# Performance work log

Hardware: AMD Instinct MI355X
Metric: run time of the kernel (lower is better)

Reference implementation:

```python
import jax, jax.numpy as jnp
import numpy as np

B, N, K = 4, 32768, 16
IN_DIM, HID, OUT_DIM = 32, 64, 32
N_DIM = 2
KIN = 2 * N_DIM + OUT_DIM  # 36
KH = 64
EPS = 1e-5


def _gelu(x):
    return jax.nn.gelu(x, approximate=False)  # torch F.gelu default (erf)


def setup_inputs() -> dict:
    key = jax.random.key(0)
    ks = jax.random.split(key, 16)
    s = lambda fan_in: 1.0 / np.sqrt(fan_in)
    return {
        "inp": jax.random.normal(ks[0], (B, N, IN_DIM), jnp.float32),
        "input_grid": jax.random.uniform(ks[1], (N, N_DIM), jnp.float32),
        "output_grid": jax.random.uniform(ks[2], (N, N_DIM), jnp.float32),
        "neighbor_idx": jax.random.randint(ks[3], (N, K), 0, N, jnp.int32),
        # pointwise projection MLP: in_dim -> hid -> out_dim, GELU between
        "Wp1": jax.random.normal(ks[4], (IN_DIM, HID), jnp.float32) * s(IN_DIM),
        "bp1": jnp.zeros((HID,), jnp.float32),
        "Wp2": jax.random.normal(ks[5], (HID, OUT_DIM), jnp.float32) * s(HID),
        "bp2": jnp.zeros((OUT_DIM,), jnp.float32),
        # per-edge kernel MLP: [2*n_dim+out_dim, 64, 64, out_dim], GELU between
        "Wk1": jax.random.normal(ks[6], (KIN, KH), jnp.float32) * s(KIN),
        "bk1": jnp.zeros((KH,), jnp.float32),
        "Wk2": jax.random.normal(ks[7], (KH, KH), jnp.float32) * s(KH),
        "bk2": jnp.zeros((KH,), jnp.float32),
        "Wk3": jax.random.normal(ks[8], (KH, OUT_DIM), jnp.float32) * s(KH),
        "bk3": jnp.zeros((OUT_DIM,), jnp.float32),
        # LayerNorm
        "ln_gamma": jnp.ones((OUT_DIM,), jnp.float32),
        "ln_beta": jnp.zeros((OUT_DIM,), jnp.float32),
    }


def reference(inp, input_grid, output_grid, neighbor_idx,
              Wp1, bp1, Wp2, bp2, Wk1, bk1, Wk2, bk2, Wk3, bk3,
              ln_gamma, ln_beta):
    # pointwise projection MLP
    x = _gelu(jnp.einsum('bnc,ch->bnh', inp, Wp1) + bp1)
    x = jnp.einsum('bnh,ho->bno', x, Wp2) + bp2  # (B, N, OUT_DIM)

    # neighbor gather (fixed K neighbors per output point)
    f_y = x[:, neighbor_idx, :]                      # (B, N, K, C)
    y_pos = input_grid[neighbor_idx]                 # (N, K, n_dim)
    x_pos = jnp.broadcast_to(output_grid[:, None, :], (N, K, N_DIM))
    pos_feat = jnp.concatenate([y_pos, x_pos], axis=-1)          # (N, K, 2*n_dim)
    agg = jnp.concatenate(
        [jnp.broadcast_to(pos_feat[None], (x.shape[0], N, K, 2 * N_DIM)), f_y],
        axis=-1)                                      # (B, N, K, KIN)

    # nonlinear kernel MLP k(x, y, f(y))
    h = _gelu(jnp.einsum('bnkc,ch->bnkh', agg, Wk1) + bk1)
    h = _gelu(jnp.einsum('bnkh,hg->bnkg', h, Wk2) + bk2)
    k_out = jnp.einsum('bnkg,go->bnko', h, Wk3) + bk3  # (B, N, K, OUT_DIM)

    # mean-aggregate over neighbors (integral transform)
    out = jnp.mean(k_out, axis=2)                      # (B, N, OUT_DIM)

    # residual (shapes match) + LayerNorm over channels
    out = out + x
    mu = jnp.mean(out, axis=-1, keepdims=True)
    var = jnp.mean((out - mu) ** 2, axis=-1, keepdims=True)
    out = (out - mu) * jax.lax.rsqrt(var + EPS) * ln_gamma + ln_beta
    return out
```

## Files before the change

### kernel.cpp

```cpp
#include <hip/hip_runtime.h>
#include <hip/hip_bf16.h>

#define BB 4
#define NN 32768
#define KKN 16
#define IN_DIM 32
#define HID 64
#define OUT_DIM 32
#define KH 64
#define WS 88
#define TOT (BB * NN)
#define NWAVES 8192
#define GTAB_N 4096

typedef __bf16 bf16;
typedef float f32x4 __attribute__((ext_vector_type(4)));
typedef bf16 bf16x8 __attribute__((ext_vector_type(8)));
typedef bf16 bf16x4 __attribute__((ext_vector_type(4)));

__device__ __forceinline__ float gelu_f(float x) {
    float x2 = x * x;
    float t  = x * fmaf(0.10294358f, x2, 2.3022082f);
    float E  = __builtin_amdgcn_exp2f(t);
    float r  = __builtin_amdgcn_rcpf(E + 1.0f);
    return fmaf(-x, r, x);
}

template <int CTRL>
__device__ __forceinline__ float dppadd(float v) {
    union { float f; int i; } u, r;
    u.f = v;
    r.i = __builtin_amdgcn_update_dpp(0, u.i, CTRL, 0xf, 0xf, true);
    return v + r.f;
}
__device__ __forceinline__ float rowsum16(float v) {
    v = dppadd<0xB1>(v);
    v = dppadd<0x4E>(v);
    v = dppadd<0x124>(v);
    v = dppadd<0x128>(v);
    return v;
}

__global__ __launch_bounds__(256) void point_mlp_kernel(
    const float* __restrict__ inp, const float* __restrict__ Wp1,
    const float* __restrict__ bp1, const float* __restrict__ Wp2,
    const float* __restrict__ bp2, bf16* __restrict__ xbf)
{
    __shared__ __align__(16) bf16 hb[4][16 * WS];
    const int tid = threadIdx.x, w = tid >> 6, lane = tid & 63;
    const int q = lane >> 4, nl = lane & 15;

    bf16x8 w1f[4];
    #pragma unroll
    for (int nb = 0; nb < 4; nb++)
        #pragma unroll
        for (int j = 0; j < 8; j++)
            w1f[nb][j] = (bf16)Wp1[(q * 8 + j) * HID + nb * 16 + nl];
    bf16x8 w2f[2][2];
    #pragma unroll
    for (int nb = 0; nb < 2; nb++)
        #pragma unroll
        for (int c = 0; c < 2; c++)
            #pragma unroll
            for (int j = 0; j < 8; j++) {
                int k = c * 32 + q * 8 + j, kp = ((k & 3) << 4) | (k >> 2);
                w2f[nb][c][j] = (bf16)Wp2[kp * OUT_DIM + nb * 16 + nl];
            }
    float b1v[4], b2v[2];
    #pragma unroll
    for (int nb = 0; nb < 4; nb++) b1v[nb] = bp1[nb * 16 + nl];
    b2v[0] = bp2[nl]; b2v[1] = bp2[16 + nl];

    const int gw = blockIdx.x * 4 + w;
    const int nw = gridDim.x * 4;

    for (int t = gw; t < TOT / 16; t += nw) {
        const int R = t * 16;
        const float* ap = inp + (size_t)(R + nl) * IN_DIM + q * 8;
        float4 av0 = *(const float4*)ap, av1 = *(const float4*)(ap + 4);
        bf16x8 af;
        af[0] = (bf16)av0.x; af[1] = (bf16)av0.y; af[2] = (bf16)av0.z; af[3] = (bf16)av0.w;
        af[4] = (bf16)av1.x; af[5] = (bf16)av1.y; af[6] = (bf16)av1.z; af[7] = (bf16)av1.w;

        f32x4 acc[4];
        #pragma unroll
        for (int nb = 0; nb < 4; nb++)
            acc[nb] = (f32x4){b1v[nb], b1v[nb], b1v[nb], b1v[nb]};
        #pragma unroll
        for (int nb = 0; nb < 4; nb++)
            acc[nb] = __builtin_amdgcn_mfma_f32_16x16x32_bf16(af, w1f[nb], acc[nb], 0, 0, 0);

        #pragma unroll
        for (int r = 0; r < 4; r++) {
            bf16x4 hv;
            #pragma unroll
            for (int nb = 0; nb < 4; nb++) hv[nb] = (bf16)gelu_f(acc[nb][r]);
            *(bf16x4*)&hb[w][(q * 4 + r) * WS + nl * 4] = hv;
        }
        bf16x8 a0 = *(const bf16x8*)&hb[w][nl * WS + q * 8];
        bf16x8 a1 = *(const bf16x8*)&hb[w][nl * WS + 32 + q * 8];
        f32x4 a2[2];
        #pragma unroll
        for (int nb = 0; nb < 2; nb++) {
            a2[nb] = (f32x4){b2v[nb], b2v[nb], b2v[nb], b2v[nb]};
            a2[nb] = __builtin_amdgcn_mfma_f32_16x16x32_bf16(a0, w2f[nb][0], a2[nb], 0, 0, 0);
            a2[nb] = __builtin_amdgcn_mfma_f32_16x16x32_bf16(a1, w2f[nb][1], a2[nb], 0, 0, 0);
        }
        #pragma unroll
        for (int r = 0; r < 4; r++)
            #pragma unroll
            for (int nb = 0; nb < 2; nb++)
                xbf[(size_t)(R + q * 4 + r) * OUT_DIM + nb * 16 + nl] = (bf16)a2[nb][r];
    }
}

__global__ __launch_bounds__(256) void gnn_edge_kernel(
    const bf16*  __restrict__ xbf,
    const float* __restrict__ igrid, const float* __restrict__ ogrid,
    const int*   __restrict__ nbi,
    const float* __restrict__ Wk1, const float* __restrict__ bk1,
    const float* __restrict__ Wk2, const float* __restrict__ bk2,
    const float* __restrict__ Wk3, const float* __restrict__ bk3,
    const float* __restrict__ gma, const float* __restrict__ bta,
    float* __restrict__ out)
{
    __shared__ __align__(16) bf16 tile[8][16 * WS];
    __shared__ __align__(16) bf16 gtab[GTAB_N];

    const int tid = threadIdx.x, w = tid >> 6, lane = tid & 63;
    const int q = lane >> 4, nl = lane & 15;
    bf16* __restrict__ TA = tile[w * 2];
    bf16* __restrict__ TB = tile[w * 2 + 1];

    for (int i = tid; i < GTAB_N; i += 256) {
        float x = (float)i * 0.0078125f - 16.0f;
        gtab[i] = (bf16)(0.5f * x * (1.0f + erff(x * 0.70710678f)));
    }

    bf16x8 w1f[4][2], w2f[4][2], w3f[2][2];
    #pragma unroll
    for (int nb = 0; nb < 4; nb++) {
        #pragma unroll
        for (int j = 0; j < 8; j++) {
            w1f[nb][0][j] = (bf16)Wk1[(4 + q * 8 + j) * KH + nb * 16 + nl];
            float v1 = 0.0f;
            if (j < 4 && q == 0) v1 = Wk1[j * KH + nb * 16 + nl];
            w1f[nb][1][j] = (bf16)v1;
        }
        #pragma unroll
        for (int c = 0; c < 2; c++)
            #pragma unroll
            for (int j = 0; j < 8; j++) {
                int k = c * 32 + q * 8 + j, kp = ((k & 3) << 4) | (k >> 2);
                w2f[nb][c][j] = (bf16)Wk2[kp * KH + nb * 16 + nl];
            }
    }
    #pragma unroll
    for (int nb = 0; nb < 2; nb++)
        #pragma unroll
        for (int c = 0; c < 2; c++)
            #pragma unroll
            for (int j = 0; j < 8; j++) {
                int k = c * 32 + q * 8 + j, kp = ((k & 3) << 4) | (k >> 2);
                w3f[nb][c][j] = (bf16)Wk3[kp * OUT_DIM + nb * 16 + nl];
            }

    float b1v[4], b2v[4], b3v[2];
    #pragma unroll
    for (int nb = 0; nb < 4; nb++) { b1v[nb] = bk1[nb * 16 + nl]; b2v[nb] = bk2[nb * 16 + nl]; }
    b3v[0] = bk3[nl]; b3v[1] = bk3[16 + nl];
    const float g0 = gma[nl], g1 = gma[16 + nl], be0 = bta[nl], be1 = bta[16 + nl];

    const int gw = blockIdx.x * 4 + w;
    const int e = lane >> 2, part = lane & 3;

    {
        const bf16x8 zf = {(bf16)0.f,(bf16)0.f,(bf16)0.f,(bf16)0.f,(bf16)0.f,(bf16)0.f,(bf16)0.f,(bf16)0.f};
        for (int i = lane * 8; i < 16 * WS; i += 64 * 8) { *(bf16x8*)&TA[i] = zf; *(bf16x8*)&TB[i] = zf; }
    }
    __syncthreads();

    #define GLUT(x) gtab[(unsigned)fminf(fmaxf(fmaf((x), 128.0f, 2048.5f), 0.0f), 4095.0f)]

    int tA = gw, tB = gw + NWAVES;
    int nA = nbi[(tA & (NN - 1)) * KKN + e];
    int nB = nbi[(tB & (NN - 1)) * KKN + e];
    uint4 fyA = ((const uint4*)(xbf + ((size_t)((tA >> 15) * NN + nA)) * OUT_DIM))[part];
    uint4 fyB = ((const uint4*)(xbf + ((size_t)((tB >> 15) * NN + nB)) * OUT_DIM))[part];
    float2 ipA, opA, ipB, opB;
    if (part == 0) {
        ipA = ((const float2*)igrid)[nA]; opA = ((const float2*)ogrid)[tA & (NN - 1)];
        ipB = ((const float2*)igrid)[nB]; opB = ((const float2*)ogrid)[tB & (NN - 1)];
    }
    bf16 xA0 = xbf[(size_t)tA * OUT_DIM + nl],      xA1 = xbf[(size_t)tA * OUT_DIM + 16 + nl];
    bf16 xB0 = xbf[(size_t)tB * OUT_DIM + nl],      xB1 = xbf[(size_t)tB * OUT_DIM + 16 + nl];

    #pragma unroll 1
    for (int it = 0; it < TOT / (2 * NWAVES); ++it) {
        *(uint4*)&TA[e * WS + part * 8] = fyA;
        *(uint4*)&TB[e * WS + part * 8] = fyB;
        if (part == 0) {
            bf16x4 pA = {(bf16)ipA.x, (bf16)ipA.y, (bf16)opA.x, (bf16)opA.y};
            bf16x4 pB = {(bf16)ipB.x, (bf16)ipB.y, (bf16)opB.x, (bf16)opB.y};
            *(bf16x4*)&TA[e * WS + 32] = pA;
            *(bf16x4*)&TB[e * WS + 32] = pB;
        }
        const float rA0 = (float)xA0, rA1 = (float)xA1, rB0 = (float)xB0, rB1 = (float)xB1;

        const int tA2 = (tA + 2 * NWAVES) & (TOT - 1);
        const int tB2 = tA2 + NWAVES;
        const int nA2 = nbi[(tA2 & (NN - 1)) * KKN + e];
        const int nB2 = nbi[(tB2 & (NN - 1)) * KKN + e];

        bf16x8 aA0 = *(const bf16x8*)&TA[nl * WS + q * 8];
        bf16x8 aA1 = *(const bf16x8*)&TA[nl * WS + 32 + q * 8];
        bf16x8 aB0 = *(const bf16x8*)&TB[nl * WS + q * 8];
        bf16x8 aB1 = *(const bf16x8*)&TB[nl * WS + 32 + q * 8];
        f32x4 cA[4], cB[4];
        #pragma unroll
        for (int nb = 0; nb < 4; nb++) {
            cA[nb] = (f32x4){b1v[nb], b1v[nb], b1v[nb], b1v[nb]};
            cB[nb] = (f32x4){b1v[nb], b1v[nb], b1v[nb], b1v[nb]};
        }
        #pragma unroll
        for (int nb = 0; nb < 4; nb++) {
            cA[nb] = __builtin_amdgcn_mfma_f32_16x16x32_bf16(aA0, w1f[nb][0], cA[nb], 0, 0, 0);
            cB[nb] = __builtin_amdgcn_mfma_f32_16x16x32_bf16(aB0, w1f[nb][0], cB[nb], 0, 0, 0);
            cA[nb] = __builtin_amdgcn_mfma_f32_16x16x32_bf16(aA1, w1f[nb][1], cA[nb], 0, 0, 0);
            cB[nb] = __builtin_amdgcn_mfma_f32_16x16x32_bf16(aB1, w1f[nb][1], cB[nb], 0, 0, 0);
        }
        #pragma unroll
        for (int r = 0; r < 4; r++) {
            bf16x4 hA, hB;
            hA[0] = GLUT(cA[0][r]);          hB[0] = GLUT(cB[0][r]);
            hA[1] = GLUT(cA[1][r]);          hB[1] = GLUT(cB[1][r]);
            hA[2] = (bf16)gelu_f(cA[2][r]);  hB[2] = (bf16)gelu_f(cB[2][r]);
            hA[3] = (bf16)gelu_f(cA[3][r]);  hB[3] = (bf16)gelu_f(cB[3][r]);
            *(bf16x4*)&TA[(q * 4 + r) * WS + nl * 4] = hA;
            *(bf16x4*)&TB[(q * 4 + r) * WS + nl * 4] = hB;
        }

        uint4 fyA2 = ((const uint4*)(xbf + ((size_t)((tA2 >> 15) * NN + nA2)) * OUT_DIM))[part];
        uint4 fyB2 = ((const uint4*)(xbf + ((size_t)((tB2 >> 15) * NN + nB2)) * OUT_DIM))[part];
        float2 ipA2, opA2, ipB2, opB2;
        if (part == 0) {
            ipA2 = ((const float2*)igrid)[nA2]; opA2 = ((const float2*)ogrid)[tA2 & (NN - 1)];
            ipB2 = ((const float2*)igrid)[nB2]; opB2 = ((const float2*)ogrid)[tB2 & (NN - 1)];
        }
        bf16 xA0n = xbf[(size_t)tA2 * OUT_DIM + nl],  xA1n = xbf[(size_t)tA2 * OUT_DIM + 16 + nl];
        bf16 xB0n = xbf[(size_t)tB2 * OUT_DIM + nl],  xB1n = xbf[(size_t)tB2 * OUT_DIM + 16 + nl];

        aA0 = *(const bf16x8*)&TA[nl * WS + q * 8];
        aA1 = *(const bf16x8*)&TA[nl * WS + 32 + q * 8];
        aB0 = *(const bf16x8*)&TB[nl * WS + q * 8];
        aB1 = *(const bf16x8*)&TB[nl * WS + 32 + q * 8];
        #pragma unroll
        for (int nb = 0; nb < 4; nb++) {
            cA[nb] = (f32x4){b2v[nb], b2v[nb], b2v[nb], b2v[nb]};
            cB[nb] = (f32x4){b2v[nb], b2v[nb], b2v[nb], b2v[nb]};
        }
        #pragma unroll
        for (int nb = 0; nb < 4; nb++) {
            cA[nb] = __builtin_amdgcn_mfma_f32_16x16x32_bf16(aA0, w2f[nb][0], cA[nb], 0, 0, 0);
            cB[nb] = __builtin_amdgcn_mfma_f32_16x16x32_bf16(aB0, w2f[nb][0], cB[nb], 0, 0, 0);
            cA[nb] = __builtin_amdgcn_mfma_f32_16x16x32_bf16(aA1, w2f[nb][1], cA[nb], 0, 0, 0);
            cB[nb] = __builtin_amdgcn_mfma_f32_16x16x32_bf16(aB1, w2f[nb][1], cB[nb], 0, 0, 0);
        }
        #pragma unroll
        for (int r = 0; r < 4; r++) {
            bf16x4 hA, hB;
            hA[0] = GLUT(cA[0][r]);          hB[0] = GLUT(cB[0][r]);
            hA[1] = GLUT(cA[1][r]);          hB[1] = GLUT(cB[1][r]);
            hA[2] = (bf16)gelu_f(cA[2][r]);  hB[2] = (bf16)gelu_f(cB[2][r]);
            hA[3] = (bf16)gelu_f(cA[3][r]);  hB[3] = (bf16)gelu_f(cB[3][r]);
            *(bf16x4*)&TA[(q * 4 + r) * WS + nl * 4] = hA;
            *(bf16x4*)&TB[(q * 4 + r) * WS + nl * 4] = hB;
        }

        aA0 = *(const bf16x8*)&TA[nl * WS + q * 8];
        aA1 = *(const bf16x8*)&TA[nl * WS + 32 + q * 8];
        aB0 = *(const bf16x8*)&TB[nl * WS + q * 8];
        aB1 = *(const bf16x8*)&TB[nl * WS + 32 + q * 8];
        f32x4 dA[2], dB[2];
        #pragma unroll
        for (int nb = 0; nb < 2; nb++) {
            dA[nb] = (f32x4){0.f, 0.f, 0.f, 0.f};
            dB[nb] = (f32x4){0.f, 0.f, 0.f, 0.f};
            dA[nb] = __builtin_amdgcn_mfma_f32_16x16x32_bf16(aA0, w3f[nb][0], dA[nb], 0, 0, 0);
            dB[nb] = __builtin_amdgcn_mfma_f32_16x16x32_bf16(aB0, w3f[nb][0], dB[nb], 0, 0, 0);
            dA[nb] = __builtin_amdgcn_mfma_f32_16x16x32_bf16(aA1, w3f[nb][1], dA[nb], 0, 0, 0);
            dB[nb] = __builtin_amdgcn_mfma_f32_16x16x32_bf16(aB1, w3f[nb][1], dB[nb], 0, 0, 0);
        }

        {
            float s0 = dA[0][0] + dA[0][1] + dA[0][2] + dA[0][3];
            float s1 = dA[1][0] + dA[1][1] + dA[1][2] + dA[1][3];
            float u0 = dB[0][0] + dB[0][1] + dB[0][2] + dB[0][3];
            float u1 = dB[1][0] + dB[1][1] + dB[1][2] + dB[1][3];
            s0 += __shfl_xor(s0, 16, 64); s0 += __shfl_xor(s0, 32, 64);
            s1 += __shfl_xor(s1, 16, 64); s1 += __shfl_xor(s1, 32, 64);
            u0 += __shfl_xor(u0, 16, 64); u0 += __shfl_xor(u0, 32, 64);
            u1 += __shfl_xor(u1, 16, 64); u1 += __shfl_xor(u1, 32, 64);

            float oA0 = s0 * 0.0625f + b3v[0] + rA0;
            float oA1 = s1 * 0.0625f + b3v[1] + rA1;
            float oB0 = u0 * 0.0625f + b3v[0] + rB0;
            float oB1 = u1 * 0.0625f + b3v[1] + rB1;

            float mA = rowsum16(oA0 + oA1) * (1.0f / 32.0f);
            float mB = rowsum16(oB0 + oB1) * (1.0f / 32.0f);
            float dA0 = oA0 - mA, dA1 = oA1 - mA, dB0 = oB0 - mB, dB1 = oB1 - mB;
            float vA = rowsum16(dA0 * dA0 + dA1 * dA1) * (1.0f / 32.0f);
            float vB = rowsum16(dB0 * dB0 + dB1 * dB1) * (1.0f / 32.0f);
            float rsA = rsqrtf(vA + 1e-5f);
            float rsB = rsqrtf(vB + 1e-5f);

            if (q == 0) {
                float* oa = out + (size_t)tA * OUT_DIM;
                float* ob = out + (size_t)tB * OUT_DIM;
                oa[nl]      = fmaf(dA0 * rsA, g0, be0);
                oa[16 + nl] = fmaf(dA1 * rsA, g1, be1);
                ob[nl]      = fmaf(dB0 * rsB, g0, be0);
                ob[16 + nl] = fmaf(dB1 * rsB, g1, be1);
            }
        }

        tA = tA2; tB = tB2;
        fyA = fyA2; fyB = fyB2;
        ipA = ipA2; opA = opA2; ipB = ipB2; opB = opB2;
        xA0 = xA0n; xA1 = xA1n; xB0 = xB0n; xB1 = xB1n;
    }
    #undef GLUT
}

extern "C" void kernel_launch(void* const* d_in, const int* in_sizes, int n_in,
                              void* d_out, int out_size, void* d_ws, size_t ws_size,
                              hipStream_t stream) {
    const float* inp   = (const float*)d_in[0];
    const float* igrid = (const float*)d_in[1];
    const float* ogrid = (const float*)d_in[2];
    const int*   nbi   = (const int*)d_in[3];
    const float* Wp1   = (const float*)d_in[4];
    const float* bp1   = (const float*)d_in[5];
    const float* Wp2   = (const float*)d_in[6];
    const float* bp2   = (const float*)d_in[7];
    const float* Wk1   = (const float*)d_in[8];
    const float* bk1   = (const float*)d_in[9];
    const float* Wk2   = (const float*)d_in[10];
    const float* bk2   = (const float*)d_in[11];
    const float* Wk3   = (const float*)d_in[12];
    const float* bk3   = (const float*)d_in[13];
    const float* gma   = (const float*)d_in[14];
    const float* bta   = (const float*)d_in[15];
    float* out = (float*)d_out;
    bf16* xbf = (bf16*)d_ws;

    point_mlp_kernel<<<1024, 256, 0, stream>>>(inp, Wp1, bp1, Wp2, bp2, xbf);
    gnn_edge_kernel<<<2048, 256, 0, stream>>>(xbf, igrid, ogrid, nbi,
                                              Wk1, bk1, Wk2, bk2, Wk3, bk3,
                                              gma, bta, out);
}
```

Baseline: 212.7 us.

## Precompute first kernel-MLP layer per source point instead of per edge

The first edge-MLP layer is linear in the concatenated [y_pos, x_pos, f_y] input, so the y_pos and f_y contributions (plus bias) are now computed once per source point in the pointwise kernel and stored as a 64-wide bf16 table. The edge kernel gathers that precomputed row, adds the x_pos term with scalar FMAs, and applies GELU, which removes one MFMA layer per edge along with the LDS staging of gathered features. In exchange, each edge gathers 128 bytes instead of 64 and the workspace gains a second table, which may make the gather more memory-bound. The first-layer pre-activation is also rounded to bf16 before GELU.

```diff
diff --git a/kernel.cpp b/kernel.cpp
--- a/kernel.cpp
+++ b/kernel.cpp
@@ -17,6 +17,7 @@
 typedef float f32x4 __attribute__((ext_vector_type(4)));
 typedef bf16 bf16x8 __attribute__((ext_vector_type(8)));
 typedef bf16 bf16x4 __attribute__((ext_vector_type(4)));
+typedef bf16 bf16x2 __attribute__((ext_vector_type(2)));
 
 __device__ __forceinline__ float gelu_f(float x) {
     float x2 = x * x;
@@ -44,7 +45,9 @@
 __global__ __launch_bounds__(256) void point_mlp_kernel(
     const float* __restrict__ inp, const float* __restrict__ Wp1,
     const float* __restrict__ bp1, const float* __restrict__ Wp2,
-    const float* __restrict__ bp2, bf16* __restrict__ xbf)
+    const float* __restrict__ bp2, const float* __restrict__ Wk1,
+    const float* __restrict__ bk1, const float* __restrict__ igrid,
+    bf16* __restrict__ xbf, bf16* __restrict__ zbf)
 {
     __shared__ __align__(16) bf16 hb[4][16 * WS];
     const int tid = threadIdx.x, w = tid >> 6, lane = tid & 63;
@@ -66,9 +69,22 @@
                 int k = c * 32 + q * 8 + j, kp = ((k & 3) << 4) | (k >> 2);
                 w2f[nb][c][j] = (bf16)Wp2[kp * OUT_DIM + nb * 16 + nl];
             }
-    float b1v[4], b2v[2];
-    #pragma unroll
-    for (int nb = 0; nb < 4; nb++) b1v[nb] = bp1[nb * 16 + nl];
+    bf16x8 wzf[4];
+    #pragma unroll
+    for (int nb = 0; nb < 4; nb++)
+        #pragma unroll
+        for (int j = 0; j < 8; j++) {
+            int p = q * 8 + j, c = (p >> 1) | ((p & 1) << 4);
+            wzf[nb][j] = (bf16)Wk1[(4 + c) * KH + nb * 16 + nl];
+        }
+    float b1v[4], b2v[2], bz[4], w1p0[4], w1p1[4];
+    #pragma unroll
+    for (int nb = 0; nb < 4; nb++) {
+        b1v[nb]  = bp1[nb * 16 + nl];
+        bz[nb]   = bk1[nb * 16 + nl];
+        w1p0[nb] = Wk1[nb * 16 + nl];
+        w1p1[nb] = Wk1[KH + nb * 16 + nl];
+    }
     b2v[0] = bp2[nl]; b2v[1] = bp2[16 + nl];
 
     const int gw = blockIdx.x * 4 + w;
@@ -107,18 +123,38 @@
             a2[nb] = __builtin_amdgcn_mfma_f32_16x16x32_bf16(a1, w2f[nb][1], a2[nb], 0, 0, 0);
         }
         #pragma unroll
-        for (int r = 0; r < 4; r++)
+        for (int r = 0; r < 4; r++) {
             #pragma unroll
             for (int nb = 0; nb < 2; nb++)
                 xbf[(size_t)(R + q * 4 + r) * OUT_DIM + nb * 16 + nl] = (bf16)a2[nb][r];
+            bf16x2 xv = { (bf16)a2[0][r], (bf16)a2[1][r] };
+            *(bf16x2*)&hb[w][(q * 4 + r) * WS + nl * 2] = xv;
+        }
+        bf16x8 az = *(const bf16x8*)&hb[w][nl * WS + q * 8];
+        f32x4 zacc[4];
+        #pragma unroll
+        for (int nb = 0; nb < 4; nb++)
+            zacc[nb] = (f32x4){bz[nb], bz[nb], bz[nb], bz[nb]};
+        #pragma unroll
+        for (int nb = 0; nb < 4; nb++)
+            zacc[nb] = __builtin_amdgcn_mfma_f32_16x16x32_bf16(az, wzf[nb], zacc[nb], 0, 0, 0);
+        #pragma unroll
+        for (int r = 0; r < 4; r++) {
+            const int row = R + q * 4 + r;
+            float2 ig = ((const float2*)igrid)[row & (NN - 1)];
+            #pragma unroll
+            for (int nb = 0; nb < 4; nb++) {
+                float zv = zacc[nb][r] + ig.x * w1p0[nb] + ig.y * w1p1[nb];
+                zbf[(size_t)row * KH + nb * 16 + nl] = (bf16)zv;
+            }
+        }
     }
 }
 
 __global__ __launch_bounds__(256) void gnn_edge_kernel(
-    const bf16*  __restrict__ xbf,
-    const float* __restrict__ igrid, const float* __restrict__ ogrid,
-    const int*   __restrict__ nbi,
-    const float* __restrict__ Wk1, const float* __restrict__ bk1,
+    const bf16*  __restrict__ xbf, const bf16* __restrict__ zbf,
+    const float* __restrict__ ogrid, const int* __restrict__ nbi,
+    const float* __restrict__ Wk1,
     const float* __restrict__ Wk2, const float* __restrict__ bk2,
     const float* __restrict__ Wk3, const float* __restrict__ bk3,
     const float* __restrict__ gma, const float* __restrict__ bta,
@@ -137,24 +173,15 @@
         gtab[i] = (bf16)(0.5f * x * (1.0f + erff(x * 0.70710678f)));
     }
 
-    bf16x8 w1f[4][2], w2f[4][2], w3f[2][2];
-    #pragma unroll
-    for (int nb = 0; nb < 4; nb++) {
-        #pragma unroll
-        for (int j = 0; j < 8; j++) {
-            w1f[nb][0][j] = (bf16)Wk1[(4 + q * 8 + j) * KH + nb * 16 + nl];
-            float v1 = 0.0f;
-            if (j < 4 && q == 0) v1 = Wk1[j * KH + nb * 16 + nl];
-            w1f[nb][1][j] = (bf16)v1;
-        }
+    bf16x8 w2f[4][2];
+    #pragma unroll
+    for (int nb = 0; nb < 4; nb++)
         #pragma unroll
         for (int c = 0; c < 2; c++)
             #pragma unroll
-            for (int j = 0; j < 8; j++) {
-                int k = c * 32 + q * 8 + j, kp = ((k & 3) << 4) | (k >> 2);
-                w2f[nb][c][j] = (bf16)Wk2[kp * KH + nb * 16 + nl];
-            }
-    }
+            for (int j = 0; j < 8; j++)
+                w2f[nb][c][j] = (bf16)Wk2[(c * 32 + q * 8 + j) * KH + nb * 16 + nl];
+    bf16x8 w3f[2][2];
     #pragma unroll
     for (int nb = 0; nb < 2; nb++)
         #pragma unroll
@@ -164,70 +191,72 @@
                 int k = c * 32 + q * 8 + j, kp = ((k & 3) << 4) | (k >> 2);
                 w3f[nb][c][j] = (bf16)Wk3[kp * OUT_DIM + nb * 16 + nl];
             }
-
-    float b1v[4], b2v[4], b3v[2];
-    #pragma unroll
-    for (int nb = 0; nb < 4; nb++) { b1v[nb] = bk1[nb * 16 + nl]; b2v[nb] = bk2[nb * 16 + nl]; }
+    float w1r2a[8], w1r2b[8], w1r3a[8], w1r3b[8];
+    #pragma unroll
+    for (int j = 0; j < 8; j++) {
+        w1r2a[j] = Wk1[2 * KH + q * 8 + j];
+        w1r2b[j] = Wk1[2 * KH + 32 + q * 8 + j];
+        w1r3a[j] = Wk1[3 * KH + q * 8 + j];
+        w1r3b[j] = Wk1[3 * KH + 32 + q * 8 + j];
+    }
+
+    float b2v[4], b3v[2];
+    #pragma unroll
+    for (int nb = 0; nb < 4; nb++) b2v[nb] = bk2[nb * 16 + nl];
     b3v[0] = bk3[nl]; b3v[1] = bk3[16 + nl];
     const float g0 = gma[nl], g1 = gma[16 + nl], be0 = bta[nl], be1 = bta[16 + nl];
 
     const int gw = blockIdx.x * 4 + w;
-    const int e = lane >> 2, part = lane & 3;
-
-    {
-        const bf16x8 zf = {(bf16)0.f,(bf16)0.f,(bf16)0.f,(bf16)0.f,(bf16)0.f,(bf16)0.f,(bf16)0.f,(bf16)0.f};
-        for (int i = lane * 8; i < 16 * WS; i += 64 * 8) { *(bf16x8*)&TA[i] = zf; *(bf16x8*)&TB[i] = zf; }
-    }
     __syncthreads();
 
     #define GLUT(x) gtab[(unsigned)fminf(fmaxf(fmaf((x), 128.0f, 2048.5f), 0.0f), 4095.0f)]
 
     int tA = gw, tB = gw + NWAVES;
-    int nA = nbi[(tA & (NN - 1)) * KKN + e];
-    int nB = nbi[(tB & (NN - 1)) * KKN + e];
-    uint4 fyA = ((const uint4*)(xbf + ((size_t)((tA >> 15) * NN + nA)) * OUT_DIM))[part];
-    uint4 fyB = ((const uint4*)(xbf + ((size_t)((tB >> 15) * NN + nB)) * OUT_DIM))[part];
-    float2 ipA, opA, ipB, opB;
-    if (part == 0) {
-        ipA = ((const float2*)igrid)[nA]; opA = ((const float2*)ogrid)[tA & (NN - 1)];
-        ipB = ((const float2*)igrid)[nB]; opB = ((const float2*)ogrid)[tB & (NN - 1)];
-    }
-    bf16 xA0 = xbf[(size_t)tA * OUT_DIM + nl],      xA1 = xbf[(size_t)tA * OUT_DIM + 16 + nl];
-    bf16 xB0 = xbf[(size_t)tB * OUT_DIM + nl],      xB1 = xbf[(size_t)tB * OUT_DIM + 16 + nl];
+    int nA = nbi[(tA & (NN - 1)) * KKN + nl];
+    int nB = nbi[(tB & (NN - 1)) * KKN + nl];
+    const bf16* zrA = zbf + ((size_t)((tA >> 15) * NN + nA)) * KH;
+    const bf16* zrB = zbf + ((size_t)((tB >> 15) * NN + nB)) * KH;
+    bf16x8 zAa = *(const bf16x8*)(zrA + q * 8), zAb = *(const bf16x8*)(zrA + 32 + q * 8);
+    bf16x8 zBa = *(const bf16x8*)(zrB + q * 8), zBb = *(const bf16x8*)(zrB + 32 + q * 8);
+    float2 ogA = ((const float2*)ogrid)[tA & (NN - 1)];
+    float2 ogB = ((const float2*)ogrid)[tB & (NN - 1)];
+    bf16 xA0 = xbf[(size_t)tA * OUT_DIM + nl], xA1 = xbf[(size_t)tA * OUT_DIM + 16 + nl];
+    bf16 xB0 = xbf[(size_t)tB * OUT_DIM + nl], xB1 = xbf[(size_t)tB * OUT_DIM + 16 + nl];
 
     #pragma unroll 1
     for (int it = 0; it < TOT / (2 * NWAVES); ++it) {
-        *(uint4*)&TA[e * WS + part * 8] = fyA;
-        *(uint4*)&TB[e * WS + part * 8] = fyB;
-        if (part == 0) {
-            bf16x4 pA = {(bf16)ipA.x, (bf16)ipA.y, (bf16)opA.x, (bf16)opA.y};
-            bf16x4 pB = {(bf16)ipB.x, (bf16)ipB.y, (bf16)opB.x, (bf16)opB.y};
-            *(bf16x4*)&TA[e * WS + 32] = pA;
-            *(bf16x4*)&TB[e * WS + 32] = pB;
-        }
         const float rA0 = (float)xA0, rA1 = (float)xA1, rB0 = (float)xB0, rB1 = (float)xB1;
+
+        bf16x8 aA0, aA1, aB0, aB1;
+        #pragma unroll
+        for (int j = 0; j < 8; j++) {
+            float pA0 = (float)zAa[j] + ogA.x * w1r2a[j] + ogA.y * w1r3a[j];
+            float pA1 = (float)zAb[j] + ogA.x * w1r2b[j] + ogA.y * w1r3b[j];
+            float pB0 = (float)zBa[j] + ogB.x * w1r2a[j] + ogB.y * w1r3a[j];
+            float pB1 = (float)zBb[j] + ogB.x * w1r2b[j] + ogB.y * w1r3b[j];
+            aA0[j] = GLUT(pA0);
+            aB0[j] = GLUT(pB0);
+            aA1[j] = (bf16)gelu_f(pA1);
+            aB1[j] = (bf16)gelu_f(pB1);
+        }
 
         const int tA2 = (tA + 2 * NWAVES) & (TOT - 1);
         const int tB2 = tA2 + NWAVES;
-        const int nA2 = nbi[(tA2 & (NN - 1)) * KKN + e];
-        const int nB2 = nbi[(tB2 & (NN - 1)) * KKN + e];
-
-        bf16x8 aA0 = *(const bf16x8*)&TA[nl * WS + q * 8];
-        bf16x8 aA1 = *(const bf16x8*)&TA[nl * WS + 32 + q * 8];
-        bf16x8 aB0 = *(const bf16x8*)&TB[nl * WS + q * 8];
-        bf16x8 aB1 = *(const bf16x8*)&TB[nl * WS + 32 + q * 8];
+        const int nA2 = nbi[(tA2 & (NN - 1)) * KKN + nl];
+        const int nB2 = nbi[(tB2 & (NN - 1)) * KKN + nl];
+
         f32x4 cA[4], cB[4];
         #pragma unroll
         for (int nb = 0; nb < 4; nb++) {
-            cA[nb] = (f32x4){b1v[nb], b1v[nb], b1v[nb], b1v[nb]};
-            cB[nb] = (f32x4){b1v[nb], b1v[nb], b1v[nb], b1v[nb]};
+            cA[nb] = (f32x4){b2v[nb], b2v[nb], b2v[nb], b2v[nb]};
+            cB[nb] = (f32x4){b2v[nb], b2v[nb], b2v[nb], b2v[nb]};
         }
         #pragma unroll
         for (int nb = 0; nb < 4; nb++) {
-            cA[nb] = __builtin_amdgcn_mfma_f32_16x16x32_bf16(aA0, w1f[nb][0], cA[nb], 0, 0, 0);
-            cB[nb] = __builtin_amdgcn_mfma_f32_16x16x32_bf16(aB0, w1f[nb][0], cB[nb], 0, 0, 0);
-            cA[nb] = __builtin_amdgcn_mfma_f32_16x16x32_bf16(aA1, w1f[nb][1], cA[nb], 0, 0, 0);
-            cB[nb] = __builtin_amdgcn_mfma_f32_16x16x32_bf16(aB1, w1f[nb][1], cB[nb], 0, 0, 0);
+            cA[nb] = __builtin_amdgcn_mfma_f32_16x16x32_bf16(aA0, w2f[nb][0], cA[nb], 0, 0, 0);
+            cB[nb] = __builtin_amdgcn_mfma_f32_16x16x32_bf16(aB0, w2f[nb][0], cB[nb], 0, 0, 0);
+            cA[nb] = __builtin_amdgcn_mfma_f32_16x16x32_bf16(aA1, w2f[nb][1], cA[nb], 0, 0, 0);
+            cB[nb] = __builtin_amdgcn_mfma_f32_16x16x32_bf16(aB1, w2f[nb][1], cB[nb], 0, 0, 0);
         }
         #pragma unroll
         for (int r = 0; r < 4; r++) {
@@ -240,56 +269,28 @@
             *(bf16x4*)&TB[(q * 4 + r) * WS + nl * 4] = hB;
         }
 
-        uint4 fyA2 = ((const uint4*)(xbf + ((size_t)((tA2 >> 15) * NN + nA2)) * OUT_DIM))[part];
-        uint4 fyB2 = ((const uint4*)(xbf + ((size_t)((tB2 >> 15) * NN + nB2)) * OUT_DIM))[part];
-        float2 ipA2, opA2, ipB2, opB2;
-        if (part == 0) {
-            ipA2 = ((const float2*)igrid)[nA2]; opA2 = ((const float2*)ogrid)[tA2 & (NN - 1)];
-            ipB2 = ((const float2*)igrid)[nB2]; opB2 = ((const float2*)ogrid)[tB2 & (NN - 1)];
-        }
-        bf16 xA0n = xbf[(size_t)tA2 * OUT_DIM + nl],  xA1n = xbf[(size_t)tA2 * OUT_DIM + 16 + nl];
-        bf16 xB0n = xbf[(size_t)tB2 * OUT_DIM + nl],  xB1n = xbf[(size_t)tB2 * OUT_DIM + 16 + nl];
-
-        aA0 = *(const bf16x8*)&TA[nl * WS + q * 8];
-        aA1 = *(const bf16x8*)&TA[nl * WS + 32 + q * 8];
-        aB0 = *(const bf16x8*)&TB[nl * WS + q * 8];
-        aB1 = *(const bf16x8*)&TB[nl * WS + 32 + q * 8];
-        #pragma unroll
-        for (int nb = 0; nb < 4; nb++) {
-            cA[nb] = (f32x4){b2v[nb], b2v[nb], b2v[nb], b2v[nb]};
-            cB[nb] = (f32x4){b2v[nb], b2v[nb], b2v[nb], b2v[nb]};
-        }
-        #pragma unroll
-        for (int nb = 0; nb < 4; nb++) {
-            cA[nb] = __builtin_amdgcn_mfma_f32_16x16x32_bf16(aA0, w2f[nb][0], cA[nb], 0, 0, 0);
-            cB[nb] = __builtin_amdgcn_mfma_f32_16x16x32_bf16(aB0, w2f[nb][0], cB[nb], 0, 0, 0);
-            cA[nb] = __builtin_amdgcn_mfma_f32_16x16x32_bf16(aA1, w2f[nb][1], cA[nb], 0, 0, 0);
-            cB[nb] = __builtin_amdgcn_mfma_f32_16x16x32_bf16(aB1, w2f[nb][1], cB[nb], 0, 0, 0);
-        }
-        #pragma unroll
-        for (int r = 0; r < 4; r++) {
-            bf16x4 hA, hB;
-            hA[0] = GLUT(cA[0][r]);          hB[0] = GLUT(cB[0][r]);
-            hA[1] = GLUT(cA[1][r]);          hB[1] = GLUT(cB[1][r]);
-            hA[2] = (bf16)gelu_f(cA[2][r]);  hB[2] = (bf16)gelu_f(cB[2][r]);
-            hA[3] = (bf16)gelu_f(cA[3][r]);  hB[3] = (bf16)gelu_f(cB[3][r]);
-            *(bf16x4*)&TA[(q * 4 + r) * WS + nl * 4] = hA;
-            *(bf16x4*)&TB[(q * 4 + r) * WS + nl * 4] = hB;
-        }
-
-        aA0 = *(const bf16x8*)&TA[nl * WS + q * 8];
-        aA1 = *(const bf16x8*)&TA[nl * WS + 32 + q * 8];
-        aB0 = *(const bf16x8*)&TB[nl * WS + q * 8];
-        aB1 = *(const bf16x8*)&TB[nl * WS + 32 + q * 8];
+        const bf16* zrA2 = zbf + ((size_t)((tA2 >> 15) * NN + nA2)) * KH;
+        const bf16* zrB2 = zbf + ((size_t)((tB2 >> 15) * NN + nB2)) * KH;
+        bf16x8 zAa2 = *(const bf16x8*)(zrA2 + q * 8), zAb2 = *(const bf16x8*)(zrA2 + 32 + q * 8);
+        bf16x8 zBa2 = *(const bf16x8*)(zrB2 + q * 8), zBb2 = *(const bf16x8*)(zrB2 + 32 + q * 8);
+        float2 ogA2 = ((const float2*)ogrid)[tA2 & (NN - 1)];
+        float2 ogB2 = ((const float2*)ogrid)[tB2 & (NN - 1)];
+        bf16 xA0n = xbf[(size_t)tA2 * OUT_DIM + nl], xA1n = xbf[(size_t)tA2 * OUT_DIM + 16 + nl];
+        bf16 xB0n = xbf[(size_t)tB2 * OUT_DIM + nl], xB1n = xbf[(size_t)tB2 * OUT_DIM + 16 + nl];
+
+        bf16x8 tA0 = *(const bf16x8*)&TA[nl * WS + q * 8];
+        bf16x8 tA1 = *(const bf16x8*)&TA[nl * WS + 32 + q * 8];
+        bf16x8 tB0 = *(const bf16x8*)&TB[nl * WS + q * 8];
+        bf16x8 tB1 = *(const bf16x8*)&TB[nl * WS + 32 + q * 8];
         f32x4 dA[2], dB[2];
         #pragma unroll
         for (int nb = 0; nb < 2; nb++) {
             dA[nb] = (f32x4){0.f, 0.f, 0.f, 0.f};
             dB[nb] = (f32x4){0.f, 0.f, 0.f, 0.f};
-            dA[nb] = __builtin_amdgcn_mfma_f32_16x16x32_bf16(aA0, w3f[nb][0], dA[nb], 0, 0, 0);
-            dB[nb] = __builtin_amdgcn_mfma_f32_16x16x32_bf16(aB0, w3f[nb][0], dB[nb], 0, 0, 0);
-            dA[nb] = __builtin_amdgcn_mfma_f32_16x16x32_bf16(aA1, w3f[nb][1], dA[nb], 0, 0, 0);
-            dB[nb] = __builtin_amdgcn_mfma_f32_16x16x32_bf16(aB1, w3f[nb][1], dB[nb], 0, 0, 0);
+            dA[nb] = __builtin_amdgcn_mfma_f32_16x16x32_bf16(tA0, w3f[nb][0], dA[nb], 0, 0, 0);
+            dB[nb] = __builtin_amdgcn_mfma_f32_16x16x32_bf16(tB0, w3f[nb][0], dB[nb], 0, 0, 0);
+            dA[nb] = __builtin_amdgcn_mfma_f32_16x16x32_bf16(tA1, w3f[nb][1], dA[nb], 0, 0, 0);
+            dB[nb] = __builtin_amdgcn_mfma_f32_16x16x32_bf16(tB1, w3f[nb][1], dB[nb], 0, 0, 0);
         }
 
         {
@@ -326,8 +327,8 @@
         }
 
         tA = tA2; tB = tB2;
-        fyA = fyA2; fyB = fyB2;
-        ipA = ipA2; opA = opA2; ipB = ipB2; opB = opB2;
+        zAa = zAa2; zAb = zAb2; zBa = zBa2; zBb = zBb2;
+        ogA = ogA2; ogB = ogB2;
         xA0 = xA0n; xA1 = xA1n; xB0 = xB0n; xB1 = xB1n;
     }
     #undef GLUT
@@ -354,9 +355,11 @@
     const float* bta   = (const float*)d_in[15];
     float* out = (float*)d_out;
     bf16* xbf = (bf16*)d_ws;
-
-    point_mlp_kernel<<<1024, 256, 0, stream>>>(inp, Wp1, bp1, Wp2, bp2, xbf);
-    gnn_edge_kernel<<<2048, 256, 0, stream>>>(xbf, igrid, ogrid, nbi,
-                                              Wk1, bk1, Wk2, bk2, Wk3, bk3,
+    bf16* zbf = xbf + (size_t)TOT * OUT_DIM;
+
+    point_mlp_kernel<<<1024, 256, 0, stream>>>(inp, Wp1, bp1, Wp2, bp2,
+                                               Wk1, bk1, igrid, xbf, zbf);
+    gnn_edge_kernel<<<2048, 256, 0, stream>>>(xbf, zbf, ogrid, nbi, Wk1,
+                                              Wk2, bk2, Wk3, bk3,
                                               gma, bta, out);
 }
```

After: 223.1 us. 4.9% more time.
